# Performance work log

Measured on AMD Instinct MI355X. Metric: run time of the kernel, lower is better.

Reference implementation:

```python
import jax, jax.numpy as jnp
import numpy as np

D_MODEL = 1024
NUM_HEADS = 16
HEAD_DIM = D_MODEL // NUM_HEADS
THETA = 10000.0
MAX_SEQ_LEN = 2048
BATCH = 4
SEQ = 2048


def _rope_tables():
    # theta_vec = 1 / theta**(arange(0, d_k, 2)/d_k), pos outer product
    inv_freq = 1.0 / (THETA ** (jnp.arange(0, HEAD_DIM, 2, dtype=jnp.float32) / HEAD_DIM))
    pos = jnp.arange(MAX_SEQ_LEN, dtype=jnp.float32)
    freqs = jnp.outer(pos, inv_freq)  # [max_seq, head_dim//2]
    return jnp.cos(freqs), jnp.sin(freqs)


def apply_rope(x, cos, sin):
    # x: [..., S, d]; cos/sin: [S, d//2]; interleaved pairwise rotation
    x1 = x[..., 0::2]
    x2 = x[..., 1::2]
    o1 = x1 * cos - x2 * sin
    o2 = x2 * cos + x1 * sin
    return jnp.stack([o1, o2], axis=-1).reshape(x.shape)


def setup_inputs() -> dict:
    key = jax.random.key(0)
    kx, kq, kk, kv, ko = jax.random.split(key, 5)
    std = (1.0 / D_MODEL) ** 0.5
    x = jax.random.normal(kx, (BATCH, SEQ, D_MODEL), dtype=jnp.float32)
    w_q = jax.random.normal(kq, (D_MODEL, D_MODEL), dtype=jnp.float32) * std
    w_k = jax.random.normal(kk, (D_MODEL, D_MODEL), dtype=jnp.float32) * std
    w_v = jax.random.normal(kv, (D_MODEL, D_MODEL), dtype=jnp.float32) * std
    w_o = jax.random.normal(ko, (D_MODEL, D_MODEL), dtype=jnp.float32) * std
    cos, sin = _rope_tables()
    return {"x": x, "w_q": w_q, "w_k": w_k, "w_v": w_v, "w_o": w_o,
            "cos": cos, "sin": sin}


def reference(x, w_q, w_k, w_v, w_o, cos, sin):
    b, s, d = x.shape
    h, dk = NUM_HEADS, HEAD_DIM

    def proj(w):
        # einsum '... s d, hd d -> ... s hd' == x @ w.T, then split heads
        y = jnp.einsum('bsd,ed->bse', x, w)
        return y.reshape(b, s, h, dk).transpose(0, 2, 1, 3)  # [b,h,s,dk]

    q = apply_rope(proj(w_q), cos[:s], sin[:s])
    k = apply_rope(proj(w_k), cos[:s], sin[:s])
    v = proj(w_v)

    scores = jnp.einsum('bhnd,bhmd->bhnm', q, k) / (dk ** 0.5)
    causal = jnp.tril(jnp.ones((s, s), dtype=bool))
    scores = jnp.where(causal, scores, -jnp.inf)
    attn = jax.nn.softmax(scores, axis=-1)
    out = jnp.einsum('bhnm,bhmd->bhnd', attn, v)  # [b,h,s,dk]
    out = out.transpose(0, 2, 1, 3).reshape(b, s, d)
    # einsum '... s hd, d hd -> ... s d' == out @ w_o.T
    return jnp.einsum('bse,de->bsd', out, w_o)
```

## Files before the change

kernel.cpp:

```cpp
#include <hip/hip_runtime.h>
#include <hip/hip_bf16.h>


typedef __bf16 bf16;
typedef __bf16 bf16x8 __attribute__((ext_vector_type(8)));
typedef __bf16 bf16x4 __attribute__((ext_vector_type(4)));
typedef float f32x4 __attribute__((ext_vector_type(4)));

#define LOG2E 1.4426950408889634f
#define QSCALE (0.125f * LOG2E * 8388608.0f)
#define SEXP_SEED ((126.94269504f - 16.0f * LOG2E) * 8388608.0f)

__device__ __forceinline__ void async16(const void* g, void* l) {
  __builtin_amdgcn_global_load_lds(
      (const __attribute__((address_space(1))) void*)g,
      (__attribute__((address_space(3))) void*)l, 16, 0, 0);
}

#define MFMA16(a, b, c) __builtin_amdgcn_mfma_f32_16x16x32_bf16(a, b, c, 0, 0, 0)

__global__ void cast_all_kernel(const float* __restrict__ x,
                                const float* __restrict__ wq,
                                const float* __restrict__ wk,
                                const float* __restrict__ wv,
                                const float* __restrict__ wo,
                                const float* __restrict__ cosT,
                                const float* __restrict__ sinT,
                                bf16* __restrict__ xb, bf16* __restrict__ wb,
                                float2* __restrict__ csT) {
  int i = blockIdx.x * blockDim.x + threadIdx.x;
  if (i >= 3145728) {
    int j = i - 3145728;
    float2 cs;
    cs.x = cosT[j];
    cs.y = sinT[j];
    csT[j] = cs;
    return;
  }
  const float* src;
  bf16* dst;
  long o;
  if (i < 2097152) {
    src = x; dst = xb; o = i;
  } else {
    long j = i - 2097152;
    int w = (int)(j >> 18);
    o = j & 262143;
    src = (w == 0) ? wq : (w == 1) ? wk : (w == 2) ? wv : wo;
    dst = wb + (long)w * 1048576;
  }
  float4 v = reinterpret_cast<const float4*>(src)[o];
  bf16x4 out;
  out.x = (bf16)v.x; out.y = (bf16)v.y; out.z = (bf16)v.z; out.w = (bf16)v.w;
  *reinterpret_cast<bf16x4*>(dst + o * 4) = out;
}

template <int EPI, int TM, int TN>
__device__ __forceinline__ void gemm_dev(const bf16* __restrict__ A,
                                         const bf16* __restrict__ B,
                                         void* __restrict__ C, int N, int K,
                                         int bm, int bn, bf16* As, bf16* Bs,
                                         const float2* __restrict__ csT) {
  constexpr int WM = TM / 64;
  constexpr int WN = 4 / WM;
  constexpr int CW = TN / WN;
  constexpr int NT = CW / 16;
  constexpr int ROUNDS = (TM + TN) / 64;
  const int tid = threadIdx.x;
  const int wid = tid >> 6, lane = tid & 63;
  const int quad = lane >> 4, l15 = lane & 15;
  const int waveM = wid / WN, waveN = wid % WN;

  f32x4 acc[4][NT] = {};
  const bf16* Ag = A + (long)bm * TM * K;
  const bf16* Bg = B + (long)bn * TN * K;

  for (int k0 = 0; k0 < K; k0 += 32) {
#pragma unroll
    for (int ri = 0; ri < ROUNDS; ++ri) {
      int c = ri * 256 + tid;
      int g = ri * 256 + (wid << 6);
      bool isA = g < TM * 4;
      int cl = isA ? c : c - TM * 4;
      int r = cl >> 2;
      int col = ((cl & 3) ^ ((r >> 1) & 3)) << 3;
      const bf16* src = (isA ? Ag : Bg) + (long)r * K + k0 + col;
      char* dst = isA ? ((char*)As + (long)g * 16)
                      : ((char*)Bs + (long)(g - TM * 4) * 16);
      async16(src, dst);
    }
    __syncthreads();
    bf16x8 af[4], bfr[NT];
#pragma unroll
    for (int t = 0; t < 4; ++t) {
      int rowA = waveM * 64 + t * 16 + l15;
      af[t] =
          *(const bf16x8*)(As + rowA * 32 + ((quad ^ ((rowA >> 1) & 3)) << 3));
    }
#pragma unroll
    for (int t = 0; t < NT; ++t) {
      int rowB = waveN * CW + t * 16 + l15;
      bfr[t] =
          *(const bf16x8*)(Bs + rowB * 32 + ((quad ^ ((rowB >> 1) & 3)) << 3));
    }
#pragma unroll
    for (int mt = 0; mt < 4; ++mt)
#pragma unroll
      for (int nt = 0; nt < NT; ++nt)
        acc[mt][nt] = MFMA16(af[mt], bfr[nt], acc[mt][nt]);
    __syncthreads();
  }

  const float qsc = (EPI == 0 && bn < 8) ? QSCALE : 1.0f;
#pragma unroll
  for (int mt = 0; mt < 4; ++mt)
#pragma unroll
    for (int nt = 0; nt < NT; ++nt)
#pragma unroll
      for (int r = 0; r < 4; ++r) {
        int row = bm * TM + waveM * 64 + mt * 16 + quad * 4 + r;
        int col = bn * TN + waveN * CW + nt * 16 + l15;
        float v = acc[mt][nt][r];
        if (EPI == 0) {
          float pr = __shfl_xor(v, 1);
          int d = col & 63;
          float2 cs = csT[(row & 2047) * 32 + (d >> 1)];
          float o =
              (col & 1) ? (v * cs.x + pr * cs.y) : (v * cs.x - pr * cs.y);
          o *= qsc;
          long off = (long)(col >> 10) * 8388608 +
                     (long)(((row >> 11) << 4) + ((col >> 6) & 15)) * 131072 +
                     (long)(row & 2047) * 64 + d;
          ((bf16*)C)[off] = (bf16)o;
        } else if (EPI == 1) {
          long off = (long)(col >> 11) * 2097152 + (long)row * 2048 +
                     (col & 2047);
          ((bf16*)C)[off] = (bf16)v;
        } else {
          ((float*)C)[(long)row * N + col] = v;
        }
      }
}

__global__ __launch_bounds__(256) void gemm_qkv(const bf16* __restrict__ xb,
                                                const bf16* __restrict__ wqk,
                                                const bf16* __restrict__ wv,
                                                bf16* __restrict__ QK,
                                                bf16* __restrict__ VT,
                                                const float2* __restrict__ csT) {
  __shared__ __align__(16) bf16 As[128 * 32];
  __shared__ __align__(16) bf16 Bs[128 * 32];
  int id = blockIdx.x;
  if (id >= 1024) {
    int v = id - 1024;
    gemm_dev<1, 64, 128>(wv, xb, VT, 8192, 1024, v >> 6, v & 63, As, Bs,
                         nullptr);
  } else {
    gemm_dev<0, 128, 128>(xb, wqk, QK, 2048, 1024, id >> 4, id & 15, As, Bs,
                          csT);
  }
}

__global__ __launch_bounds__(256) void gemm_out(const bf16* __restrict__ A,
                                                const bf16* __restrict__ B,
                                                float* __restrict__ C) {
  __shared__ __align__(16) bf16 As[128 * 32];
  __shared__ __align__(16) bf16 Bs[64 * 32];
  gemm_dev<2, 128, 64>(A, B, C, 1024, 1024, blockIdx.y, blockIdx.x, As, Bs,
                       nullptr);
}

__device__ __forceinline__ void attn_step(const bf16* Ks, const bf16* Vs,
                                          bf16* Pw, const bf16x8* qf,
                                          const bf16x8 ones, f32x4* accO,
                                          f32x4& accL, int quad, int l15,
                                          int qloc, bool diag) {
  const int sw = l15 & 7;
  const f32x4 seedv = {SEXP_SEED, SEXP_SEED, SEXP_SEED, SEXP_SEED};
  f32x4 sacc[4] = {seedv, seedv, seedv, seedv};
#pragma unroll
  for (int mt = 0; mt < 4; ++mt)
#pragma unroll
    for (int kk = 0; kk < 2; ++kk) {
      bf16x8 kf = *(const bf16x8*)(Ks + (mt * 16 + l15) * 64 +
                                   ((((kk << 2) + quad) ^ sw) << 3));
      sacc[mt] = MFMA16(kf, qf[kk], sacc[mt]);
    }
  if (diag) {
#pragma unroll
    for (int mt = 0; mt < 4; ++mt)
#pragma unroll
      for (int r = 0; r < 4; ++r)
        if ((mt * 16 + quad * 4 + r) > qloc) sacc[mt][r] = 0.0f;
  }
#pragma unroll
  for (int mt = 0; mt < 4; ++mt) {
    int i0 = (int)sacc[mt][0], i1 = (int)sacc[mt][1];
    int i2 = (int)sacc[mt][2], i3 = (int)sacc[mt][3];
    uint2 pk;
    pk.x = __builtin_amdgcn_perm((unsigned)i1, (unsigned)i0, 0x07060302u);
    pk.y = __builtin_amdgcn_perm((unsigned)i3, (unsigned)i2, 0x07060302u);
    *(uint2*)(Pw + l15 * 88 + mt * 16 + quad * 4) = pk;
  }
  asm volatile("s_waitcnt lgkmcnt(0)" ::: "memory");
  bf16x8 pfr[2];
#pragma unroll
  for (int kk = 0; kk < 2; ++kk)
    pfr[kk] = *(const bf16x8*)(Pw + l15 * 88 + kk * 32 + quad * 8);
#pragma unroll
  for (int nt = 0; nt < 4; ++nt)
#pragma unroll
    for (int kk = 0; kk < 2; ++kk) {
      bf16x8 vf = *(const bf16x8*)(Vs + (nt * 16 + l15) * 64 +
                                   ((((kk << 2) + quad) ^ sw) << 3));
      accO[nt] = MFMA16(pfr[kk], vf, accO[nt]);
    }
#pragma unroll
  for (int kk = 0; kk < 2; ++kk)
    accL = MFMA16(pfr[kk], ones, accL);
}

__global__ __launch_bounds__(256, 4) void attn_kernel(
    const bf16* __restrict__ Q, const bf16* __restrict__ Kg,
    const bf16* __restrict__ VT, bf16* __restrict__ Out) {
  __shared__ __align__(16) bf16 Ks[64 * 64];
  __shared__ __align__(16) bf16 Vs[64 * 64];
  __shared__ __align__(16) bf16 Ps[4][16 * 88];
  const int tid = threadIdx.x, wid = tid >> 6, lane = tid & 63;
  const int quad = lane >> 4, l15 = lane & 15;
  const int p = blockIdx.x, bh = blockIdx.y;
  const int q0t = p, q1t = 31 - p;
  const bf16* Qb = Q + (long)bh * 131072;
  const bf16* Kb = Kg + (long)bh * 131072;
  const bf16* Vb = VT + (long)bh * 131072;
  bf16* Pw = &Ps[wid][0];
  const int qloc = wid * 16 + l15;

  bf16x8 ones;
#pragma unroll
  for (int j = 0; j < 8; ++j) ones[j] = (bf16)1.0f;

  bf16x8 qf0[2], qf1[2];
#pragma unroll
  for (int kk = 0; kk < 2; ++kk) {
    qf0[kk] = *(const bf16x8*)(Qb + (long)(q0t * 64 + qloc) * 64 + kk * 32 +
                               quad * 8);
    qf1[kk] = *(const bf16x8*)(Qb + (long)(q1t * 64 + qloc) * 64 + kk * 32 +
                               quad * 8);
  }
  f32x4 acc0[4] = {}, acc1[4] = {};
  f32x4 accL0 = {}, accL1 = {};

  for (int kt = 0; kt <= q1t; ++kt) {
#pragma unroll
    for (int it = 0; it < 2; ++it) {
      int chunk = it * 256 + tid;
      int r = chunk >> 3;
      int c = (((chunk & 7) ^ (r & 7)) << 3);
      int ldsbase = (it * 256 + wid * 64) * 16;
      async16(Kb + (long)(kt * 64 + r) * 64 + c, (char*)Ks + ldsbase);
      async16(Vb + (long)r * 2048 + kt * 64 + c, (char*)Vs + ldsbase);
    }
    __syncthreads();
    attn_step(Ks, Vs, Pw, qf1, ones, acc1, accL1, quad, l15, qloc, kt == q1t);
    if (kt <= q0t)
      attn_step(Ks, Vs, Pw, qf0, ones, acc0, accL0, quad, l15, qloc,
                kt == q0t);
    __syncthreads();
  }

  const int b = bh >> 4, h = bh & 15;
#pragma unroll
  for (int r = 0; r < 4; ++r) {
    float lr0 = 1.0f / accL0[r];
    float lr1 = 1.0f / accL1[r];
#pragma unroll
    for (int nt = 0; nt < 4; ++nt) {
      int d = h * 64 + nt * 16 + l15;
      int qg0 = q0t * 64 + wid * 16 + quad * 4 + r;
      int qg1 = q1t * 64 + wid * 16 + quad * 4 + r;
      Out[(long)(b * 2048 + qg0) * 1024 + d] = (bf16)(acc0[nt][r] * lr0);
      Out[(long)(b * 2048 + qg1) * 1024 + d] = (bf16)(acc1[nt][r] * lr1);
    }
  }
}

extern "C" void kernel_launch(void* const* d_in, const int* in_sizes, int n_in,
                              void* d_out, int out_size, void* d_ws,
                              size_t ws_size, hipStream_t stream) {
  const float* x = (const float*)d_in[0];
  const float* w_q = (const float*)d_in[1];
  const float* w_k = (const float*)d_in[2];
  const float* w_v = (const float*)d_in[3];
  const float* w_o = (const float*)d_in[4];
  const float* cosT = (const float*)d_in[5];
  const float* sinT = (const float*)d_in[6];

  char* ws = (char*)d_ws;
  bf16* xb = (bf16*)(ws + 0);
  bf16* wqb = (bf16*)(ws + 16777216);
  bf16* wvb = (bf16*)(ws + 20971520);
  bf16* wob = (bf16*)(ws + 23068672);
  bf16* Qb = (bf16*)(ws + 25165824);
  bf16* Kb = (bf16*)(ws + 41943040);
  bf16* VTb = (bf16*)(ws + 58720256);
  float2* csT = (float2*)(ws + 75497472);
  bf16* attnb = xb;

  cast_all_kernel<<<12544, 256, 0, stream>>>(x, w_q, w_k, w_v, w_o, cosT,
                                             sinT, xb, wqb, csT);

  gemm_qkv<<<2048, 256, 0, stream>>>(xb, wqb, wvb, Qb, VTb, csT);

  attn_kernel<<<dim3(16, 64), 256, 0, stream>>>(Qb, Kb, VTb, attnb);

  gemm_out<<<dim3(16, 64), 256, 0, stream>>>(attnb, wob, (float*)d_out);
}
```

Baseline: 276.6 us.

## Double-buffer GEMM LDS tiles and remap QKV block order across XCDs

The shared GEMM routine now keeps two LDS buffers. It issues the async global-to-LDS loads for the next K-slice before running the MFMAs on the current one, and drops one barrier per iteration. The goal is to hide global load latency behind matrix math. In exchange, LDS use per block doubles, which may lower occupancy. The QKV launch also permutes block IDs with a stride-8 mapping, intended to keep neighbouring tiles on the same XCD for better L2 reuse.

```diff
diff --git a/kernel.cpp b/kernel.cpp
--- a/kernel.cpp
+++ b/kernel.cpp
@@ -75,7 +75,7 @@
   const bf16* Ag = A + (long)bm * TM * K;
   const bf16* Bg = B + (long)bn * TN * K;
 
-  for (int k0 = 0; k0 < K; k0 += 32) {
+  auto stage = [&](int buf, int k0) {
 #pragma unroll
     for (int ri = 0; ri < ROUNDS; ++ri) {
       int c = ri * 256 + tid;
@@ -85,30 +85,43 @@
       int r = cl >> 2;
       int col = ((cl & 3) ^ ((r >> 1) & 3)) << 3;
       const bf16* src = (isA ? Ag : Bg) + (long)r * K + k0 + col;
-      char* dst = isA ? ((char*)As + (long)g * 16)
-                      : ((char*)Bs + (long)(g - TM * 4) * 16);
+      char* dst = isA ? ((char*)As + (long)buf * (TM * 64) + (long)g * 16)
+                      : ((char*)Bs + (long)buf * (TN * 64) +
+                         (long)(g - TM * 4) * 16);
       async16(src, dst);
     }
-    __syncthreads();
+  };
+
+  stage(0, 0);
+  __syncthreads();
+  int cur = 0;
+  for (int k0 = 0; k0 < K; k0 += 32) {
+    const bool more = (k0 + 32) < K;
+    if (more) stage(cur ^ 1, k0 + 32);
+    const bf16* Asb = As + cur * (TM * 32);
+    const bf16* Bsb = Bs + cur * (TN * 32);
     bf16x8 af[4], bfr[NT];
 #pragma unroll
     for (int t = 0; t < 4; ++t) {
       int rowA = waveM * 64 + t * 16 + l15;
       af[t] =
-          *(const bf16x8*)(As + rowA * 32 + ((quad ^ ((rowA >> 1) & 3)) << 3));
+          *(const bf16x8*)(Asb + rowA * 32 + ((quad ^ ((rowA >> 1) & 3)) << 3));
     }
 #pragma unroll
     for (int t = 0; t < NT; ++t) {
       int rowB = waveN * CW + t * 16 + l15;
       bfr[t] =
-          *(const bf16x8*)(Bs + rowB * 32 + ((quad ^ ((rowB >> 1) & 3)) << 3));
+          *(const bf16x8*)(Bsb + rowB * 32 + ((quad ^ ((rowB >> 1) & 3)) << 3));
     }
 #pragma unroll
     for (int mt = 0; mt < 4; ++mt)
 #pragma unroll
       for (int nt = 0; nt < NT; ++nt)
         acc[mt][nt] = MFMA16(af[mt], bfr[nt], acc[mt][nt]);
-    __syncthreads();
+    if (more) {
+      __syncthreads();
+      cur ^= 1;
+    }
   }
 
   const float qsc = (EPI == 0 && bn < 8) ? QSCALE : 1.0f;
@@ -148,15 +161,17 @@
                                                 bf16* __restrict__ QK,
                                                 bf16* __restrict__ VT,
                                                 const float2* __restrict__ csT) {
-  __shared__ __align__(16) bf16 As[128 * 32];
-  __shared__ __align__(16) bf16 Bs[128 * 32];
-  int id = blockIdx.x;
-  if (id >= 1024) {
-    int v = id - 1024;
-    gemm_dev<1, 64, 128>(wv, xb, VT, 8192, 1024, v >> 6, v & 63, As, Bs,
+  __shared__ __align__(16) bf16 As[2 * 128 * 32];
+  __shared__ __align__(16) bf16 Bs[2 * 128 * 32];
+  int p = blockIdx.x;
+  if (p >= 1024) {
+    int pv = p - 1024;
+    int lv = (pv & 7) * 128 + (pv >> 3);
+    gemm_dev<1, 64, 128>(wv, xb, VT, 8192, 1024, lv & 15, lv >> 4, As, Bs,
                          nullptr);
   } else {
-    gemm_dev<0, 128, 128>(xb, wqk, QK, 2048, 1024, id >> 4, id & 15, As, Bs,
+    int l = (p & 7) * 128 + (p >> 3);
+    gemm_dev<0, 128, 128>(xb, wqk, QK, 2048, 1024, l >> 4, l & 15, As, Bs,
                           csT);
   }
 }
@@ -164,8 +179,8 @@
 __global__ __launch_bounds__(256) void gemm_out(const bf16* __restrict__ A,
                                                 const bf16* __restrict__ B,
                                                 float* __restrict__ C) {
-  __shared__ __align__(16) bf16 As[128 * 32];
-  __shared__ __align__(16) bf16 Bs[64 * 32];
+  __shared__ __align__(16) bf16 As[2 * 128 * 32];
+  __shared__ __align__(16) bf16 Bs[2 * 64 * 32];
   gemm_dev<2, 128, 64>(A, B, C, 1024, 1024, blockIdx.y, blockIdx.x, As, Bs,
                        nullptr);
 }
```

New measurement: 276.0 us. About the same (-0.2%).
